# Optimization experiments

Hardware: AMD Instinct MI355X
Metric: run time of the kernel (lower is better)

Reference implementation:

```python
import jax, jax.numpy as jnp
import numpy as np

N_NODES = 100000
N_EDGES = 1600000
NODE_NF = 11   # num_node_fs
EDGE_NF = 4    # edges_nf
H_NF = 128     # h_nf
EMB_NF = 4     # emb_nf


def _linear_params(k, fan_in, fan_out):
    # torch nn.Linear default init: U(-1/sqrt(fan_in), 1/sqrt(fan_in))
    lim = 1.0 / np.sqrt(fan_in)
    kw, kb = jax.random.split(k)
    W = jax.random.uniform(kw, (fan_in, fan_out), minval=-lim, maxval=lim, dtype=jnp.float32)
    b = jax.random.uniform(kb, (fan_out,), minval=-lim, maxval=lim, dtype=jnp.float32)
    return W, b


def setup_inputs() -> dict:
    key = jax.random.key(0)
    ks = jax.random.split(key, 8)
    node_feats = jax.random.normal(ks[0], (N_NODES, NODE_NF), dtype=jnp.float32)
    edge_index = jax.random.randint(ks[1], (2, N_EDGES), 0, N_NODES, dtype=jnp.int32)
    edge_attr = jax.random.normal(ks[2], (N_EDGES, EDGE_NF), dtype=jnp.float32)
    # NELayer edge MLP: Linear(2*in_nf+edges_nf, h_nf) -> ReLU -> Linear(h_nf, h_nf) -> ReLU
    eW1, eb1 = _linear_params(ks[3], 2 * NODE_NF + EDGE_NF, H_NF)
    eW2, eb2 = _linear_params(ks[4], H_NF, H_NF)
    # NELayer node MLP: Linear(in_nf+h_nf, h_nf) -> ReLU -> Linear(h_nf, out_nf=h_nf)
    nW1, nb1 = _linear_params(ks[5], NODE_NF + H_NF, H_NF)
    nW2, nb2 = _linear_params(ks[6], H_NF, H_NF)
    # fc_emb: Linear(h_nf, emb_nf)
    fW, fb = _linear_params(ks[7], H_NF, EMB_NF)
    return dict(node_feats=node_feats, edge_index=edge_index, edge_attr=edge_attr,
                eW1=eW1, eb1=eb1, eW2=eW2, eb2=eb2,
                nW1=nW1, nb1=nb1, nW2=nW2, nb2=nb2, fW=fW, fb=fb)


def reference(node_feats, edge_index, edge_attr,
              eW1, eb1, eW2, eb2, nW1, nb1, nW2, nb2, fW, fb):
    row, col = edge_index[0], edge_index[1]          # [E], [E]
    src = node_feats[row]                            # [E, NODE_NF] gather
    dst = node_feats[col]                            # [E, NODE_NF] gather
    # edge model
    e_in = jnp.concatenate([src, dst, edge_attr], axis=1)   # [E, 2*NODE_NF+EDGE_NF]
    e_h = jax.nn.relu(e_in @ eW1 + eb1)
    edge_feats = jax.nn.relu(e_h @ eW2 + eb2)                # [E, H_NF]
    # node model: scatter-sum edge feats to source nodes
    agg = jax.ops.segment_sum(edge_feats, row, num_segments=node_feats.shape[0])  # [N, H_NF]
    n_in = jnp.concatenate([node_feats, agg], axis=1)        # [N, NODE_NF+H_NF]
    n_h = jax.nn.relu(n_in @ nW1 + nb1)
    h = n_h @ nW2 + nb2                                      # [N, H_NF]
    # embedding head
    return h @ fW + fb                                       # [N, EMB_NF]
```

## Files before the change

### kernel.cpp

```cpp
#include <hip/hip_runtime.h>

#define N_NODES 100000
#define N_EDGES 1600000
#define NODE_NF 11
#define EDGE_NF 4
#define H_NF 128
#define SCAN_B 1024
#define NBLK ((N_NODES + SCAN_B - 1) / SCAN_B)

#define K1P 40
#define K2P 136
#define EFP 131
#define K1N 160

typedef _Float16 half8 __attribute__((ext_vector_type(8)));
typedef float floatx4 __attribute__((ext_vector_type(4)));

__device__ inline half8 load8f(const float* p) {
    float4 x0 = *(const float4*)(p);
    float4 x1 = *(const float4*)(p + 4);
    half8 r;
    r[0]=(_Float16)x0.x; r[1]=(_Float16)x0.y; r[2]=(_Float16)x0.z; r[3]=(_Float16)x0.w;
    r[4]=(_Float16)x1.x; r[5]=(_Float16)x1.y; r[6]=(_Float16)x1.z; r[7]=(_Float16)x1.w;
    return r;
}
__device__ inline half8 zero8() {
    half8 z;
    #pragma unroll
    for (int j = 0; j < 8; ++j) z[j] = (_Float16)0.f;
    return z;
}

#define SEG0 (N_NODES * 12)
#define SEG1 (SEG0 + H_NF * K1P)
#define SEG2 (SEG1 + H_NF * K2P)
#define SEG3 (SEG2 + H_NF * K1N)
#define SEG4 (SEG3 + 16 * K2P + 4)
#define SEG5 (SEG4 + N_EDGES)

__global__ __launch_bounds__(256)
void prep_hist_kernel(const float* __restrict__ nf,
                      const float* __restrict__ eW1,
                      const float* __restrict__ eW2,
                      const float* __restrict__ nW1,
                      const float* __restrict__ nW2,
                      const float* __restrict__ fW,
                      const float* __restrict__ nb2,
                      const float* __restrict__ fb,
                      const int*   __restrict__ edge_index,
                      _Float16* __restrict__ nfh,
                      _Float16* __restrict__ w1h,
                      _Float16* __restrict__ w2h,
                      _Float16* __restrict__ w1nh,
                      _Float16* __restrict__ w23h,
                      float* __restrict__ b23,
                      int* hist)
{
    int i = blockIdx.x * 256 + threadIdx.x;
    if (i < SEG0) {
        int n = i / 12, k = i - n * 12;
        nfh[i] = (k < NODE_NF) ? (_Float16)nf[(size_t)n * NODE_NF + k] : (_Float16)0.f;
    } else if (i < SEG1) {
        int j = i - SEG0;
        int n = j / K1P, k = j - n * K1P;
        float v = 0.f;
        if (k < 11)                 v = eW1[k * H_NF + n];
        else if (k >= 12 && k < 23) v = eW1[(k - 1) * H_NF + n];
        else if (k >= 24 && k < 28) v = eW1[(k - 2) * H_NF + n];
        w1h[j] = (_Float16)v;
    } else if (i < SEG2) {
        int j = i - SEG1;
        int n = j / K2P, k = j - n * K2P;
        w2h[j] = (k < H_NF) ? (_Float16)eW2[k * H_NF + n] : (_Float16)0.f;
    } else if (i < SEG3) {
        int j = i - SEG2;
        int n = j / K1N, k = j - n * K1N;
        float v = 0.f;
        if (k < 11)                  v = nW1[k * H_NF + n];
        else if (k >= 12 && k < 140) v = nW1[(k - 1) * H_NF + n];
        w1nh[j] = (_Float16)v;
    } else if (i < SEG4) {
        int j = i - SEG3;
        if (j < 16 * K2P) {
            int n = j / K2P, k = j - n * K2P;
            float v = 0.f;
            if (n < 4 && k < H_NF) {
                for (int q = 0; q < H_NF; ++q) v += nW2[k * H_NF + q] * fW[q * 4 + n];
            }
            w23h[j] = (_Float16)v;
        } else {
            int o = j - 16 * K2P;
            float v = fb[o];
            for (int q = 0; q < H_NF; ++q) v += nb2[q] * fW[q * 4 + o];
            b23[o] = v;
        }
    } else if (i < SEG5) {
        int e = i - SEG4;
        atomicAdd(&hist[edge_index[e]], 1);
    }
}

__global__ __launch_bounds__(256)
void transpose_w2(const float* __restrict__ W, float* __restrict__ WT) {
    int i = blockIdx.x * 256 + threadIdx.x;
    if (i < H_NF * H_NF) {
        int k = i >> 7, j = i & (H_NF - 1);
        WT[j * H_NF + k] = W[i];
    }
}

__global__ __launch_bounds__(SCAN_B)
void scan1_kernel(const int* __restrict__ hist, int* starts, int* bsum) {
    __shared__ int buf[SCAN_B];
    int i = blockIdx.x * SCAN_B + threadIdx.x;
    int v = (i < N_NODES) ? hist[i] : 0;
    buf[threadIdx.x] = v;
    __syncthreads();
    for (int off = 1; off < SCAN_B; off <<= 1) {
        int t = (threadIdx.x >= off) ? buf[threadIdx.x - off] : 0;
        __syncthreads();
        buf[threadIdx.x] += t;
        __syncthreads();
    }
    if (i < N_NODES) starts[i] = buf[threadIdx.x] - v;
    if (threadIdx.x == SCAN_B - 1) bsum[blockIdx.x] = buf[SCAN_B - 1];
}

__global__ void scan2_kernel(int* bsum) {
    if (threadIdx.x == 0 && blockIdx.x == 0) {
        int run = 0;
        for (int b = 0; b < NBLK; ++b) { int t = bsum[b]; bsum[b] = run; run += t; }
        bsum[NBLK] = run;
    }
}

__global__ __launch_bounds__(256)
void scan3_kernel(int* starts, int* cursor, const int* __restrict__ bsum) {
    int i = blockIdx.x * 256 + threadIdx.x;
    if (i < N_NODES) {
        int s = starts[i] + bsum[i / SCAN_B];
        starts[i] = s;
        cursor[i] = s;
    }
    if (i == 0) starts[N_NODES] = bsum[NBLK];
}

__global__ __launch_bounds__(256)
void permrec_kernel(const int* __restrict__ edge_index,
                    const float* __restrict__ edge_attr,
                    int* cursor,
                    int4* __restrict__ rec)
{
    int e = blockIdx.x * 256 + threadIdx.x;
    if (e >= N_EDGES) return;
    int row = edge_index[e];
    int col = edge_index[N_EDGES + e];
    float4 a4 = ((const float4*)edge_attr)[e];
    union { _Float16 h[4]; int2 v; } u;
    u.h[0] = (_Float16)a4.x; u.h[1] = (_Float16)a4.y;
    u.h[2] = (_Float16)a4.z; u.h[3] = (_Float16)a4.w;
    int pos = atomicAdd(&cursor[row], 1);
    rec[pos] = make_int4(row, col, u.v.x, u.v.y);
}

__global__ __launch_bounds__(256)
void permute_kernel(const int* __restrict__ edge_index, int* cursor, int* perm) {
    int e = blockIdx.x * 256 + threadIdx.x;
    if (e < N_EDGES) {
        int pos = atomicAdd(&cursor[edge_index[e]], 1);
        perm[pos] = e;
    }
}

#define E_ARENA_SZ 5504

__global__ __launch_bounds__(256, 2)
void edge_mfma_kernel(const int4* __restrict__ recs,
                      const _Float16* __restrict__ nfh,
                      const _Float16* __restrict__ w1h,
                      const float* __restrict__ eb1,
                      const _Float16* __restrict__ w2h,
                      const float* __restrict__ eb2,
                      float* agg)
{
    __shared__ __align__(16) char smem[4 * E_ARENA_SZ];
    int t = threadIdx.x;
    int wv = t >> 6, lane = t & 63;
    char* arena = smem + wv * E_ARENA_SZ;
    _Float16* Ain = (_Float16*)arena;
    _Float16* Hs  = (_Float16*)(arena + 1024);
    int m = lane & 15, quad = lane >> 4;

    half8 w1f[8], w2f[8][4];
    #pragma unroll
    for (int tile = 0; tile < 8; ++tile)
        w1f[tile] = *(const half8*)(w1h + (tile * 16 + m) * K1P + quad * 8);
    #pragma unroll
    for (int tile = 0; tile < 8; ++tile)
        #pragma unroll
        for (int ks = 0; ks < 4; ++ks)
            w2f[tile][ks] = *(const half8*)(w2h + (tile * 16 + m) * K2P + ks * 32 + quad * 8);
    float b1v[8], b2v[8];
    #pragma unroll
    for (int tile = 0; tile < 8; ++tile) {
        b1v[tile] = eb1[tile * 16 + m];
        b2v[tile] = eb2[tile * 16 + m];
    }

    const int nwin = N_EDGES / 16;
    const int STRIDE = gridDim.x * 4;
    int win = blockIdx.x * 4 + wv;
    if (win >= nwin) return;

    int4 rc = recs[win * 16 + m];
    int2 g0 = make_int2(0, 0), g1 = g0, g2 = g0;
    if (quad < 2) {
        int node = (quad == 0) ? rc.x : rc.y;
        const int2* p = (const int2*)(nfh + (size_t)node * 12);
        g0 = p[0]; g1 = p[1]; g2 = p[2];
    }

    while (true) {
        int next = win + STRIDE;
        bool hn = next < nwin;
        int4 rcn = make_int4(0, 0, 0, 0);
        if (hn) rcn = recs[next * 16 + m];

        _Float16* arow = Ain + m * 32;
        if (quad == 0) {
            ((int2*)arow)[0] = g0; ((int2*)arow)[1] = g1; ((int2*)arow)[2] = g2;
        } else if (quad == 1) {
            int2* d = (int2*)(arow + 12);
            d[0] = g0; d[1] = g1; d[2] = g2;
        } else if (quad == 2) {
            int2* d = (int2*)(arow + 24);
            d[0] = make_int2(rc.z, rc.w);
            d[1] = make_int2(0, 0);
        }

        half8 a1 = *(const half8*)(Ain + m * 32 + quad * 8);

        #pragma unroll
        for (int tile = 0; tile < 8; ++tile) {
            floatx4 c = {0.f, 0.f, 0.f, 0.f};
            c = __builtin_amdgcn_mfma_f32_16x16x32_f16(a1, w1f[tile], c, 0, 0, 0);
            int n = tile * 16 + m;
            #pragma unroll
            for (int r = 0; r < 4; ++r)
                Hs[(quad * 4 + r) * K2P + n] = (_Float16)fmaxf(c[r] + b1v[tile], 0.f);
        }

        half8 a2[4];
        #pragma unroll
        for (int ks = 0; ks < 4; ++ks)
            a2[ks] = *(const half8*)(Hs + m * K2P + ks * 32 + quad * 8);

        float vals[32];
        #pragma unroll
        for (int tile = 0; tile < 8; ++tile) {
            floatx4 c = {0.f, 0.f, 0.f, 0.f};
            #pragma unroll
            for (int ks = 0; ks < 4; ++ks)
                c = __builtin_amdgcn_mfma_f32_16x16x32_f16(a2[ks], w2f[tile][ks], c, 0, 0, 0);
            #pragma unroll
            for (int r = 0; r < 4; ++r)
                vals[tile * 4 + r] = fmaxf(c[r] + b2v[tile], 0.f);
        }

        int2 n0 = make_int2(0, 0), n1 = n0, n2 = n0;
        if (hn && quad < 2) {
            int node = (quad == 0) ? rcn.x : rcn.y;
            const int2* p = (const int2*)(nfh + (size_t)node * 12);
            n0 = p[0]; n1 = p[1]; n2 = p[2];
        }

        int row = rc.x;
        int rprev = __shfl(row, lane - 1);
        bool bi = (lane < 16) && (m == 0 || rprev != row);
        unsigned long long bm = __ballot(bi);
        unsigned mk = (unsigned)(bm & 0xFFFFull);
        int er0 = __shfl(row, quad * 4 + 0);
        int er1 = __shfl(row, quad * 4 + 1);
        int er2 = __shfl(row, quad * 4 + 2);
        int er3 = __shfl(row, quad * 4 + 3);
        while (mk) {
            int start = __builtin_ctz(mk);
            mk &= mk - 1;
            int srow = __shfl(row, start);
            float s[8];
            #pragma unroll
            for (int tile = 0; tile < 8; ++tile) {
                float v = 0.f;
                if (er0 == srow) v += vals[tile * 4 + 0];
                if (er1 == srow) v += vals[tile * 4 + 1];
                if (er2 == srow) v += vals[tile * 4 + 2];
                if (er3 == srow) v += vals[tile * 4 + 3];
                s[tile] = v;
            }
            #pragma unroll
            for (int tile = 0; tile < 8; ++tile) {
                s[tile] += __shfl_xor(s[tile], 16);
                s[tile] += __shfl_xor(s[tile], 32);
            }
            if (quad == 0) {
                #pragma unroll
                for (int tile = 0; tile < 8; ++tile)
                    unsafeAtomicAdd(&agg[(size_t)srow * H_NF + tile * 16 + m], s[tile]);
            }
        }

        if (!hn) break;
        win = next; rc = rcn; g0 = n0; g1 = n1; g2 = n2;
    }
}

#define G_W1      0
#define G_W2      10240
#define G_ARENA   45056
#define G_ARENA_SZ 8448
#define G_TOTAL   (G_ARENA + 4 * G_ARENA_SZ)

__global__ __launch_bounds__(256, 2)
void edge_mfma_gather_kernel(const _Float16* __restrict__ nfh,
                             const int*   __restrict__ edge_index,
                             const float* __restrict__ edge_attr,
                             const _Float16* __restrict__ w1h,
                             const float* __restrict__ eb1,
                             const _Float16* __restrict__ w2h,
                             const float* __restrict__ eb2,
                             const int*   __restrict__ perm,
                             float* agg)
{
    __shared__ __align__(16) char smem[G_TOTAL];
    _Float16* W1s = (_Float16*)(smem + G_W1);
    _Float16* W2s = (_Float16*)(smem + G_W2);
    int t = threadIdx.x;
    {
        const float4* g1 = (const float4*)w1h;
        float4* s1 = (float4*)W1s;
        for (int i = t; i < 640; i += 256) s1[i] = g1[i];
        const float4* g2 = (const float4*)w2h;
        float4* s2 = (float4*)W2s;
        for (int i = t; i < 2176; i += 256) s2[i] = g2[i];
    }
    __syncthreads();

    int wv = t >> 6, lane = t & 63;
    char* arena = smem + G_ARENA + wv * G_ARENA_SZ;
    _Float16* Ain  = (_Float16*)arena;
    _Float16* Hs   = (_Float16*)(arena + 1280);
    float*    efS  = (float*)arena;
    int*      rowsS = (int*)(arena + 8384);

    int m = lane & 15, quad = lane >> 4;
    int el = lane & 15, grp = lane >> 4;
    _Float16* arow = Ain + el * K1P;

    float b1v[8], b2v[8];
    #pragma unroll
    for (int tile = 0; tile < 8; ++tile) {
        b1v[tile] = eb1[tile * 16 + m];
        b2v[tile] = eb2[tile * 16 + m];
    }

    const int nwin = N_EDGES / 16;
    for (int win = blockIdx.x * 4 + wv; win < nwin; win += gridDim.x * 4) {
        int e = perm[win * 16 + el];
        if (grp < 2) {
            int node = edge_index[grp * N_EDGES + e];
            const int2* p = (const int2*)(nfh + (size_t)node * 12);
            int2 x0 = p[0], x1 = p[1], x2 = p[2];
            char* dst = (char*)(arow + grp * 12);
            *(int2*)(dst) = x0; *(int2*)(dst + 8) = x1; *(int2*)(dst + 16) = x2;
        } else if (grp == 2) {
            float4 a4 = ((const float4*)edge_attr)[e];
            arow[24] = (_Float16)a4.x; arow[25] = (_Float16)a4.y;
            arow[26] = (_Float16)a4.z; arow[27] = (_Float16)a4.w;
        } else {
            rowsS[el] = edge_index[e];
            *(int2*)((char*)arow + 56) = make_int2(0, 0);
        }

        half8 a1 = *(const half8*)(Ain + m * K1P + quad * 8);
        #pragma unroll
        for (int tile = 0; tile < 8; ++tile) {
            half8 b = *(const half8*)(W1s + (tile * 16 + m) * K1P + quad * 8);
            floatx4 c = {0.f, 0.f, 0.f, 0.f};
            c = __builtin_amdgcn_mfma_f32_16x16x32_f16(a1, b, c, 0, 0, 0);
            int n = tile * 16 + m;
            #pragma unroll
            for (int r = 0; r < 4; ++r)
                Hs[(quad * 4 + r) * K2P + n] = (_Float16)fmaxf(c[r] + b1v[tile], 0.f);
        }
        half8 a2[4];
        #pragma unroll
        for (int ks = 0; ks < 4; ++ks)
            a2[ks] = *(const half8*)(Hs + m * K2P + ks * 32 + quad * 8);
        #pragma unroll
        for (int tile = 0; tile < 8; ++tile) {
            floatx4 c = {0.f, 0.f, 0.f, 0.f};
            #pragma unroll
            for (int ks = 0; ks < 4; ++ks) {
                half8 b = *(const half8*)(W2s + (tile * 16 + m) * K2P + ks * 32 + quad * 8);
                c = __builtin_amdgcn_mfma_f32_16x16x32_f16(a2[ks], b, c, 0, 0, 0);
            }
            #pragma unroll
            for (int r = 0; r < 4; ++r)
                efS[(quad * 4 + r) * EFP + tile * 16 + m] = fmaxf(c[r] + b2v[tile], 0.f);
        }

        int f = lane;
        int cur = rowsS[0];
        float acc0 = efS[f], acc1 = efS[64 + f];
        #pragma unroll 1
        for (int i = 1; i < 16; ++i) {
            int r = rowsS[i];
            float v0 = efS[i * EFP + f];
            float v1 = efS[i * EFP + 64 + f];
            if (r != cur) {
                unsafeAtomicAdd(&agg[(size_t)cur * H_NF + f], acc0);
                unsafeAtomicAdd(&agg[(size_t)cur * H_NF + 64 + f], acc1);
                acc0 = v0; acc1 = v1; cur = r;
            } else { acc0 += v0; acc1 += v1; }
        }
        unsafeAtomicAdd(&agg[(size_t)cur * H_NF + f], acc0);
        unsafeAtomicAdd(&agg[(size_t)cur * H_NF + 64 + f], acc1);
    }
}

#define N_W1    0
#define N_W23   40960
#define N_HS    45312

__global__ __launch_bounds__(256, 2)
void node_mfma_kernel(const float* __restrict__ node_feats,
                      const float* __restrict__ agg,
                      const _Float16* __restrict__ w1nh,
                      const float* __restrict__ nb1,
                      const _Float16* __restrict__ w23h,
                      const float* __restrict__ b23,
                      float* __restrict__ out)
{
    __shared__ __align__(16) char smem[N_HS + 4 * 4352];
    _Float16* W1N  = (_Float16*)(smem + N_W1);
    _Float16* W23s = (_Float16*)(smem + N_W23);
    int t = threadIdx.x;
    {
        const float4* g1 = (const float4*)w1nh;
        float4* s1 = (float4*)W1N;
        for (int i = t; i < 2560; i += 256) s1[i] = g1[i];
        const float4* g2 = (const float4*)w23h;
        float4* s2 = (float4*)W23s;
        for (int i = t; i < 272; i += 256) s2[i] = g2[i];
    }
    __syncthreads();

    int wv = t >> 6, lane = t & 63;
    int m = lane & 15, quad = lane >> 4;
    _Float16* HsW = (_Float16*)(smem + N_HS + wv * 4352);
    const int ntile = (N_NODES + 63) / 64;

    float nb1v[8];
    #pragma unroll
    for (int tile = 0; tile < 8; ++tile) nb1v[tile] = nb1[tile * 16 + m];
    float b23v = (m < 4) ? b23[m] : 0.f;

    for (int ti = blockIdx.x; ti < ntile; ti += gridDim.x) {
        int nb = (ti * 4 + wv) * 16;
        if (nb >= N_NODES) continue;
        int nodeA = nb + m;
        if (nodeA >= N_NODES) nodeA = N_NODES - 1;
        const float* ag  = agg + (size_t)nodeA * H_NF;
        const float* nfp = node_feats + (size_t)nodeA * NODE_NF;

        half8 afr[5];
        if (quad == 0) {
            half8 r;
            #pragma unroll
            for (int j = 0; j < 8; ++j) r[j] = (_Float16)nfp[j];
            afr[0] = r;
            afr[4] = load8f(ag + 116);
        } else if (quad == 1) {
            half8 r;
            r[0] = (_Float16)nfp[8]; r[1] = (_Float16)nfp[9];
            r[2] = (_Float16)nfp[10]; r[3] = (_Float16)0.f;
            float4 x = *(const float4*)(ag);
            r[4] = (_Float16)x.x; r[5] = (_Float16)x.y;
            r[6] = (_Float16)x.z; r[7] = (_Float16)x.w;
            afr[0] = r;
            float4 y = *(const float4*)(ag + 124);
            half8 s = zero8();
            s[0] = (_Float16)y.x; s[1] = (_Float16)y.y;
            s[2] = (_Float16)y.z; s[3] = (_Float16)y.w;
            afr[4] = s;
        } else if (quad == 2) {
            afr[0] = load8f(ag + 4);
            afr[4] = zero8();
        } else {
            afr[0] = load8f(ag + 12);
            afr[4] = zero8();
        }
        afr[1] = load8f(ag + 20 + 8 * quad);
        afr[2] = load8f(ag + 52 + 8 * quad);
        afr[3] = load8f(ag + 84 + 8 * quad);

        #pragma unroll
        for (int tile = 0; tile < 8; ++tile) {
            floatx4 c = {0.f, 0.f, 0.f, 0.f};
            #pragma unroll
            for (int ks = 0; ks < 5; ++ks) {
                half8 b = *(const half8*)(W1N + (tile * 16 + m) * K1N + ks * 32 + quad * 8);
                c = __builtin_amdgcn_mfma_f32_16x16x32_f16(afr[ks], b, c, 0, 0, 0);
            }
            #pragma unroll
            for (int r = 0; r < 4; ++r)
                HsW[(quad * 4 + r) * K2P + tile * 16 + m] = (_Float16)fmaxf(c[r] + nb1v[tile], 0.f);
        }

        half8 a2[4];
        #pragma unroll
        for (int ks = 0; ks < 4; ++ks)
            a2[ks] = *(const half8*)(HsW + m * K2P + ks * 32 + quad * 8);
        floatx4 c23 = {0.f, 0.f, 0.f, 0.f};
        #pragma unroll
        for (int ks = 0; ks < 4; ++ks) {
            half8 b = *(const half8*)(W23s + m * K2P + ks * 32 + quad * 8);
            c23 = __builtin_amdgcn_mfma_f32_16x16x32_f16(a2[ks], b, c23, 0, 0, 0);
        }
        if (m < 4) {
            #pragma unroll
            for (int r = 0; r < 4; ++r) {
                int node = nb + quad * 4 + r;
                if (node < N_NODES) out[node * 4 + m] = c23[r] + b23v;
            }
        }
    }
}

__global__ __launch_bounds__(256)
void edge_kernel_atomic(const float* __restrict__ node_feats,
                        const int*   __restrict__ edge_index,
                        const float* __restrict__ edge_attr,
                        const float* __restrict__ eW1,
                        const float* __restrict__ eb1,
                        const float* __restrict__ W2T,
                        const float* __restrict__ eb2,
                        float* agg)
{
    int e = blockIdx.x * 256 + threadIdx.x;
    if (e >= N_EDGES) return;
    int row = edge_index[e];
    int col = edge_index[N_EDGES + e];
    float h[H_NF];
    #pragma unroll
    for (int j = 0; j < H_NF; ++j) h[j] = eb1[j];
    const float* srcp = node_feats + (size_t)row * NODE_NF;
    #pragma unroll 1
    for (int k = 0; k < NODE_NF; ++k) {
        float x = srcp[k];
        const float* w = eW1 + k * H_NF;
        #pragma unroll
        for (int j = 0; j < H_NF; ++j) h[j] = fmaf(x, w[j], h[j]);
    }
    const float* dstp = node_feats + (size_t)col * NODE_NF;
    #pragma unroll 1
    for (int k = 0; k < NODE_NF; ++k) {
        float x = dstp[k];
        const float* w = eW1 + (NODE_NF + k) * H_NF;
        #pragma unroll
        for (int j = 0; j < H_NF; ++j) h[j] = fmaf(x, w[j], h[j]);
    }
    float4 at = ((const float4*)edge_attr)[e];
    float av[EDGE_NF] = {at.x, at.y, at.z, at.w};
    #pragma unroll
    for (int k = 0; k < EDGE_NF; ++k) {
        float x = av[k];
        const float* w = eW1 + (2 * NODE_NF + k) * H_NF;
        #pragma unroll
        for (int j = 0; j < H_NF; ++j) h[j] = fmaf(x, w[j], h[j]);
    }
    #pragma unroll
    for (int j = 0; j < H_NF; ++j) h[j] = fmaxf(h[j], 0.f);
    #pragma unroll 1
    for (int j0 = 0; j0 < H_NF; j0 += 8) {
        float acc[8];
        #pragma unroll
        for (int jj = 0; jj < 8; ++jj) acc[jj] = eb2[j0 + jj];
        #pragma unroll
        for (int k = 0; k < H_NF; ++k) {
            float x = h[k];
            #pragma unroll
            for (int jj = 0; jj < 8; ++jj)
                acc[jj] = fmaf(x, W2T[(j0 + jj) * H_NF + k], acc[jj]);
        }
        #pragma unroll
        for (int jj = 0; jj < 8; ++jj)
            unsafeAtomicAdd(&agg[(size_t)row * H_NF + j0 + jj], fmaxf(acc[jj], 0.f));
    }
}

__global__ __launch_bounds__(256)
void node_kernel1(const float* __restrict__ node_feats, float* agg_nh,
                  const float* __restrict__ nW1, const float* __restrict__ nb1)
{
    int n = blockIdx.x * 256 + threadIdx.x;
    if (n >= N_NODES) return;
    float acc[H_NF];
    #pragma unroll
    for (int j = 0; j < H_NF; ++j) acc[j] = nb1[j];
    const float* nfp = node_feats + (size_t)n * NODE_NF;
    #pragma unroll 1
    for (int k = 0; k < NODE_NF; ++k) {
        float x = nfp[k];
        const float* w = nW1 + k * H_NF;
        #pragma unroll
        for (int j = 0; j < H_NF; ++j) acc[j] = fmaf(x, w[j], acc[j]);
    }
    const float4* ap = (const float4*)(agg_nh + (size_t)n * H_NF);
    #pragma unroll 1
    for (int k4 = 0; k4 < H_NF / 4; ++k4) {
        float4 x = ap[k4];
        const float* w0 = nW1 + (NODE_NF + k4 * 4 + 0) * H_NF;
        const float* w1 = nW1 + (NODE_NF + k4 * 4 + 1) * H_NF;
        const float* w2 = nW1 + (NODE_NF + k4 * 4 + 2) * H_NF;
        const float* w3 = nW1 + (NODE_NF + k4 * 4 + 3) * H_NF;
        #pragma unroll
        for (int j = 0; j < H_NF; ++j) {
            acc[j] = fmaf(x.x, w0[j], acc[j]);
            acc[j] = fmaf(x.y, w1[j], acc[j]);
            acc[j] = fmaf(x.z, w2[j], acc[j]);
            acc[j] = fmaf(x.w, w3[j], acc[j]);
        }
    }
    float* op = agg_nh + (size_t)n * H_NF;
    #pragma unroll
    for (int j4 = 0; j4 < H_NF / 4; ++j4) {
        float4 o = make_float4(fmaxf(acc[j4*4+0], 0.f), fmaxf(acc[j4*4+1], 0.f),
                               fmaxf(acc[j4*4+2], 0.f), fmaxf(acc[j4*4+3], 0.f));
        ((float4*)op)[j4] = o;
    }
}

__global__ __launch_bounds__(256)
void node_kernel2(const float* __restrict__ nh, const float* __restrict__ nW2,
                  const float* __restrict__ nb2, const float* __restrict__ fW,
                  const float* __restrict__ fb, float* __restrict__ out)
{
    int n = blockIdx.x * 256 + threadIdx.x;
    if (n >= N_NODES) return;
    float acc[H_NF];
    #pragma unroll
    for (int j = 0; j < H_NF; ++j) acc[j] = nb2[j];
    const float4* hp = (const float4*)(nh + (size_t)n * H_NF);
    #pragma unroll 1
    for (int k4 = 0; k4 < H_NF / 4; ++k4) {
        float4 x = hp[k4];
        const float* w0 = nW2 + (k4 * 4 + 0) * H_NF;
        const float* w1 = nW2 + (k4 * 4 + 1) * H_NF;
        const float* w2 = nW2 + (k4 * 4 + 2) * H_NF;
        const float* w3 = nW2 + (k4 * 4 + 3) * H_NF;
        #pragma unroll
        for (int j = 0; j < H_NF; ++j) {
            acc[j] = fmaf(x.x, w0[j], acc[j]);
            acc[j] = fmaf(x.y, w1[j], acc[j]);
            acc[j] = fmaf(x.z, w2[j], acc[j]);
            acc[j] = fmaf(x.w, w3[j], acc[j]);
        }
    }
    float o0 = fb[0], o1 = fb[1], o2 = fb[2], o3 = fb[3];
    #pragma unroll
    for (int j = 0; j < H_NF; ++j) {
        o0 = fmaf(acc[j], fW[j * 4 + 0], o0);
        o1 = fmaf(acc[j], fW[j * 4 + 1], o1);
        o2 = fmaf(acc[j], fW[j * 4 + 2], o2);
        o3 = fmaf(acc[j], fW[j * 4 + 3], o3);
    }
    ((float4*)out)[n] = make_float4(o0, o1, o2, o3);
}

extern "C" void kernel_launch(void* const* d_in, const int* in_sizes, int n_in,
                              void* d_out, int out_size, void* d_ws, size_t ws_size,
                              hipStream_t stream)
{
    const float* node_feats = (const float*)d_in[0];
    const int*   edge_index = (const int*)d_in[1];
    const float* edge_attr  = (const float*)d_in[2];
    const float* eW1 = (const float*)d_in[3];
    const float* eb1 = (const float*)d_in[4];
    const float* eW2 = (const float*)d_in[5];
    const float* eb2 = (const float*)d_in[6];
    const float* nW1 = (const float*)d_in[7];
    const float* nb1 = (const float*)d_in[8];
    const float* nW2 = (const float*)d_in[9];
    const float* nb2 = (const float*)d_in[10];
    const float* fW  = (const float*)d_in[11];
    const float* fb  = (const float*)d_in[12];
    float* out = (float*)d_out;

    size_t off = 0;
    auto carve = [&](size_t bytes) {
        void* p = (char*)d_ws + off;
        off = (off + bytes + 255) & ~(size_t)255;
        return p;
    };
    float*     agg    = (float*)carve((size_t)N_NODES * H_NF * sizeof(float));
    int*       hist   = (int*)  carve((size_t)N_NODES * sizeof(int));
    size_t zero_bytes = off;
    int*       starts = (int*)  carve((size_t)(N_NODES + 1) * sizeof(int));
    int*       cursor = (int*)  carve((size_t)N_NODES * sizeof(int));
    int*       bsum   = (int*)  carve((size_t)(NBLK + 1) * sizeof(int));
    _Float16*  nfh    = (_Float16*)carve((size_t)N_NODES * 12 * sizeof(_Float16));
    _Float16*  w1h    = (_Float16*)carve((size_t)H_NF * K1P * sizeof(_Float16));
    _Float16*  w2h    = (_Float16*)carve((size_t)H_NF * K2P * sizeof(_Float16));
    _Float16*  w1nh   = (_Float16*)carve((size_t)H_NF * K1N * sizeof(_Float16));
    _Float16*  w23h   = (_Float16*)carve((size_t)16 * K2P * sizeof(_Float16));
    float*     b23    = (float*)carve(4 * sizeof(float));
    int*       perm   = (int*)  carve((size_t)N_EDGES * sizeof(int));
    size_t required_t2 = off;
    int4*      rec    = (int4*) carve((size_t)N_EDGES * sizeof(int4));
    size_t required_t1 = off;

    if (ws_size >= required_t2) {
        hipMemsetAsync(d_ws, 0, zero_bytes, stream);
        prep_hist_kernel<<<(SEG5 + 255) / 256, 256, 0, stream>>>(
            node_feats, eW1, eW2, nW1, nW2, fW, nb2, fb, edge_index,
            nfh, w1h, w2h, w1nh, w23h, b23, hist);
        scan1_kernel<<<NBLK, SCAN_B, 0, stream>>>(hist, starts, bsum);
        scan2_kernel<<<1, 64, 0, stream>>>(bsum);
        scan3_kernel<<<(N_NODES + 255) / 256, 256, 0, stream>>>(starts, cursor, bsum);

        if (ws_size >= required_t1) {
            permrec_kernel<<<(N_EDGES + 255) / 256, 256, 0, stream>>>(
                edge_index, edge_attr, cursor, rec);
            edge_mfma_kernel<<<512, 256, 0, stream>>>(
                rec, nfh, w1h, eb1, w2h, eb2, agg);
        } else {
            permute_kernel<<<(N_EDGES + 255) / 256, 256, 0, stream>>>(edge_index, cursor, perm);
            edge_mfma_gather_kernel<<<512, 256, 0, stream>>>(
                nfh, edge_index, edge_attr, w1h, eb1, w2h, eb2, perm, agg);
        }
        node_mfma_kernel<<<512, 256, 0, stream>>>(
            node_feats, agg, w1nh, nb1, w23h, b23, out);
    } else {
        float* agg_fb = (float*)d_ws;
        float* W2T_fb = (float*)((char*)d_ws + (size_t)N_NODES * H_NF * sizeof(float));
        transpose_w2<<<(H_NF * H_NF + 255) / 256, 256, 0, stream>>>(eW2, W2T_fb);
        hipMemsetAsync(agg_fb, 0, (size_t)N_NODES * H_NF * sizeof(float), stream);
        edge_kernel_atomic<<<(N_EDGES + 255) / 256, 256, 0, stream>>>(
            node_feats, edge_index, edge_attr, eW1, eb1, W2T_fb, eb2, agg_fb);
        node_kernel1<<<(N_NODES + 255) / 256, 256, 0, stream>>>(node_feats, agg_fb, nW1, nb1);
        node_kernel2<<<(N_NODES + 255) / 256, 256, 0, stream>>>(agg_fb, nW2, nb2, fW, fb, out);
    }
}
```

Baseline: 426.9 us.

## Split second edge-MLP layer across waves to cut registers and raise occupancy

Each wave now holds only two of the eight second-layer weight tiles. The four waves share their first-layer hidden activations through double-buffered LDS with a block barrier, and each wave computes its 32 output columns for all four windows. Fewer weight registers allow three blocks per CU and a 768-block grid. The cost is a __syncthreads per iteration, extra LDS traffic and an atomic scatter loop repeated per window.

```diff
diff --git a/kernel.cpp b/kernel.cpp
--- a/kernel.cpp
+++ b/kernel.cpp
@@ -172,9 +172,7 @@
     }
 }
 
-#define E_ARENA_SZ 5504
-
-__global__ __launch_bounds__(256, 2)
+__global__ __launch_bounds__(256, 3)
 void edge_mfma_kernel(const int4* __restrict__ recs,
                       const _Float16* __restrict__ nfh,
                       const _Float16* __restrict__ w1h,
@@ -183,88 +181,101 @@
                       const float* __restrict__ eb2,
                       float* agg)
 {
-    __shared__ __align__(16) char smem[4 * E_ARENA_SZ];
+    __shared__ __align__(16) char smem[4 * 1024 + 8 * 4352];
     int t = threadIdx.x;
     int wv = t >> 6, lane = t & 63;
-    char* arena = smem + wv * E_ARENA_SZ;
-    _Float16* Ain = (_Float16*)arena;
-    _Float16* Hs  = (_Float16*)(arena + 1024);
+    _Float16* Ain = (_Float16*)(smem + wv * 1024);
+    char* hsbase = smem + 4096;
     int m = lane & 15, quad = lane >> 4;
 
-    half8 w1f[8], w2f[8][4];
+    half8 w1f[8], w2f[2][4];
     #pragma unroll
     for (int tile = 0; tile < 8; ++tile)
         w1f[tile] = *(const half8*)(w1h + (tile * 16 + m) * K1P + quad * 8);
     #pragma unroll
-    for (int tile = 0; tile < 8; ++tile)
+    for (int tt = 0; tt < 2; ++tt)
         #pragma unroll
         for (int ks = 0; ks < 4; ++ks)
-            w2f[tile][ks] = *(const half8*)(w2h + (tile * 16 + m) * K2P + ks * 32 + quad * 8);
-    float b1v[8], b2v[8];
-    #pragma unroll
-    for (int tile = 0; tile < 8; ++tile) {
-        b1v[tile] = eb1[tile * 16 + m];
-        b2v[tile] = eb2[tile * 16 + m];
-    }
+            w2f[tt][ks] = *(const half8*)(w2h + ((wv * 2 + tt) * 16 + m) * K2P + ks * 32 + quad * 8);
+    float b1v[8], b2v[2];
+    #pragma unroll
+    for (int tile = 0; tile < 8; ++tile) b1v[tile] = eb1[tile * 16 + m];
+    #pragma unroll
+    for (int tt = 0; tt < 2; ++tt) b2v[tt] = eb2[(wv * 2 + tt) * 16 + m];
 
     const int nwin = N_EDGES / 16;
     const int STRIDE = gridDim.x * 4;
-    int win = blockIdx.x * 4 + wv;
-    if (win >= nwin) return;
-
-    int4 rc = recs[win * 16 + m];
+    int base = blockIdx.x * 4;
+    int win = base + wv;
+
+    int4 rc = make_int4(0, 0, 0, 0);
+    if (win < nwin) rc = recs[win * 16 + m];
     int2 g0 = make_int2(0, 0), g1 = g0, g2 = g0;
-    if (quad < 2) {
+    if (win < nwin && quad < 2) {
         int node = (quad == 0) ? rc.x : rc.y;
         const int2* p = (const int2*)(nfh + (size_t)node * 12);
         g0 = p[0]; g1 = p[1]; g2 = p[2];
     }
 
-    while (true) {
+    int buf = 0;
+    for (; base < nwin; base += STRIDE, win += STRIDE) {
+        bool hw = win < nwin;
         int next = win + STRIDE;
         bool hn = next < nwin;
         int4 rcn = make_int4(0, 0, 0, 0);
         if (hn) rcn = recs[next * 16 + m];
 
-        _Float16* arow = Ain + m * 32;
-        if (quad == 0) {
-            ((int2*)arow)[0] = g0; ((int2*)arow)[1] = g1; ((int2*)arow)[2] = g2;
-        } else if (quad == 1) {
-            int2* d = (int2*)(arow + 12);
-            d[0] = g0; d[1] = g1; d[2] = g2;
-        } else if (quad == 2) {
-            int2* d = (int2*)(arow + 24);
-            d[0] = make_int2(rc.z, rc.w);
-            d[1] = make_int2(0, 0);
-        }
-
-        half8 a1 = *(const half8*)(Ain + m * 32 + quad * 8);
-
-        #pragma unroll
-        for (int tile = 0; tile < 8; ++tile) {
-            floatx4 c = {0.f, 0.f, 0.f, 0.f};
-            c = __builtin_amdgcn_mfma_f32_16x16x32_f16(a1, w1f[tile], c, 0, 0, 0);
-            int n = tile * 16 + m;
-            #pragma unroll
-            for (int r = 0; r < 4; ++r)
-                Hs[(quad * 4 + r) * K2P + n] = (_Float16)fmaxf(c[r] + b1v[tile], 0.f);
-        }
-
-        half8 a2[4];
-        #pragma unroll
-        for (int ks = 0; ks < 4; ++ks)
-            a2[ks] = *(const half8*)(Hs + m * K2P + ks * 32 + quad * 8);
-
-        float vals[32];
-        #pragma unroll
-        for (int tile = 0; tile < 8; ++tile) {
-            floatx4 c = {0.f, 0.f, 0.f, 0.f};
-            #pragma unroll
-            for (int ks = 0; ks < 4; ++ks)
-                c = __builtin_amdgcn_mfma_f32_16x16x32_f16(a2[ks], w2f[tile][ks], c, 0, 0, 0);
-            #pragma unroll
-            for (int r = 0; r < 4; ++r)
-                vals[tile * 4 + r] = fmaxf(c[r] + b2v[tile], 0.f);
+        int rowj[4];
+        #pragma unroll
+        for (int j = 0; j < 4; ++j)
+            rowj[j] = (base + j < nwin) ? ((const int*)recs)[(base + j) * 64 + m * 4] : -1;
+
+        if (hw) {
+            _Float16* arow = Ain + m * 32;
+            if (quad == 0) {
+                ((int2*)arow)[0] = g0; ((int2*)arow)[1] = g1; ((int2*)arow)[2] = g2;
+            } else if (quad == 1) {
+                int2* d = (int2*)(arow + 12);
+                d[0] = g0; d[1] = g1; d[2] = g2;
+            } else if (quad == 2) {
+                int2* d = (int2*)(arow + 24);
+                d[0] = make_int2(rc.z, rc.w);
+                d[1] = make_int2(0, 0);
+            }
+            half8 a1 = *(const half8*)(Ain + m * 32 + quad * 8);
+            _Float16* Hs = (_Float16*)(hsbase + (buf * 4 + wv) * 4352);
+            #pragma unroll
+            for (int tile = 0; tile < 8; ++tile) {
+                floatx4 c = {0.f, 0.f, 0.f, 0.f};
+                c = __builtin_amdgcn_mfma_f32_16x16x32_f16(a1, w1f[tile], c, 0, 0, 0);
+                int n = tile * 16 + m;
+                #pragma unroll
+                for (int r = 0; r < 4; ++r)
+                    Hs[(quad * 4 + r) * K2P + n] = (_Float16)fmaxf(c[r] + b1v[tile], 0.f);
+            }
+        }
+        __syncthreads();
+
+        float vals[4][8];
+        #pragma unroll
+        for (int j = 0; j < 4; ++j) {
+            if (base + j < nwin) {
+                const _Float16* Hj = (const _Float16*)(hsbase + (buf * 4 + j) * 4352);
+                half8 a2[4];
+                #pragma unroll
+                for (int ks = 0; ks < 4; ++ks)
+                    a2[ks] = *(const half8*)(Hj + m * K2P + ks * 32 + quad * 8);
+                #pragma unroll
+                for (int tt = 0; tt < 2; ++tt) {
+                    floatx4 c = {0.f, 0.f, 0.f, 0.f};
+                    #pragma unroll
+                    for (int ks = 0; ks < 4; ++ks)
+                        c = __builtin_amdgcn_mfma_f32_16x16x32_f16(a2[ks], w2f[tt][ks], c, 0, 0, 0);
+                    #pragma unroll
+                    for (int r = 0; r < 4; ++r)
+                        vals[j][tt * 4 + r] = fmaxf(c[r] + b2v[tt], 0.f);
+                }
+            }
         }
 
         int2 n0 = make_int2(0, 0), n1 = n0, n2 = n0;
@@ -274,43 +285,39 @@
             n0 = p[0]; n1 = p[1]; n2 = p[2];
         }
 
-        int row = rc.x;
-        int rprev = __shfl(row, lane - 1);
-        bool bi = (lane < 16) && (m == 0 || rprev != row);
-        unsigned long long bm = __ballot(bi);
-        unsigned mk = (unsigned)(bm & 0xFFFFull);
-        int er0 = __shfl(row, quad * 4 + 0);
-        int er1 = __shfl(row, quad * 4 + 1);
-        int er2 = __shfl(row, quad * 4 + 2);
-        int er3 = __shfl(row, quad * 4 + 3);
-        while (mk) {
-            int start = __builtin_ctz(mk);
-            mk &= mk - 1;
-            int srow = __shfl(row, start);
-            float s[8];
-            #pragma unroll
-            for (int tile = 0; tile < 8; ++tile) {
-                float v = 0.f;
-                if (er0 == srow) v += vals[tile * 4 + 0];
-                if (er1 == srow) v += vals[tile * 4 + 1];
-                if (er2 == srow) v += vals[tile * 4 + 2];
-                if (er3 == srow) v += vals[tile * 4 + 3];
-                s[tile] = v;
+        #pragma unroll
+        for (int j = 0; j < 4; ++j) {
+            if (base + j < nwin) {
+                int row = rowj[j];
+                int rprev = __shfl(row, lane - 1);
+                bool bi = (lane < 16) && (m == 0 || rprev != row);
+                unsigned long long bm = __ballot(bi);
+                unsigned mk = (unsigned)(bm & 0xFFFFull);
+                int er0 = __shfl(row, quad * 4 + 0);
+                int er1 = __shfl(row, quad * 4 + 1);
+                int er2 = __shfl(row, quad * 4 + 2);
+                int er3 = __shfl(row, quad * 4 + 3);
+                while (mk) {
+                    int start = __builtin_ctz(mk);
+                    mk &= mk - 1;
+                    int srow = __shfl(row, start);
+                    float s0 = 0.f, s1 = 0.f;
+                    if (er0 == srow) { s0 += vals[j][0]; s1 += vals[j][4]; }
+                    if (er1 == srow) { s0 += vals[j][1]; s1 += vals[j][5]; }
+                    if (er2 == srow) { s0 += vals[j][2]; s1 += vals[j][6]; }
+                    if (er3 == srow) { s0 += vals[j][3]; s1 += vals[j][7]; }
+                    s0 += __shfl_xor(s0, 16); s0 += __shfl_xor(s0, 32);
+                    s1 += __shfl_xor(s1, 16); s1 += __shfl_xor(s1, 32);
+                    if (quad == 0) {
+                        unsafeAtomicAdd(&agg[(size_t)srow * H_NF + (wv * 2 + 0) * 16 + m], s0);
+                        unsafeAtomicAdd(&agg[(size_t)srow * H_NF + (wv * 2 + 1) * 16 + m], s1);
+                    }
+                }
             }
-            #pragma unroll
-            for (int tile = 0; tile < 8; ++tile) {
-                s[tile] += __shfl_xor(s[tile], 16);
-                s[tile] += __shfl_xor(s[tile], 32);
-            }
-            if (quad == 0) {
-                #pragma unroll
-                for (int tile = 0; tile < 8; ++tile)
-                    unsafeAtomicAdd(&agg[(size_t)srow * H_NF + tile * 16 + m], s[tile]);
-            }
-        }
-
-        if (!hn) break;
-        win = next; rc = rcn; g0 = n0; g1 = n1; g2 = n2;
+        }
+
+        rc = rcn; g0 = n0; g1 = n1; g2 = n2;
+        buf ^= 1;
     }
 }
 
@@ -732,7 +739,7 @@
         if (ws_size >= required_t1) {
             permrec_kernel<<<(N_EDGES + 255) / 256, 256, 0, stream>>>(
                 edge_index, edge_attr, cursor, rec);
-            edge_mfma_kernel<<<512, 256, 0, stream>>>(
+            edge_mfma_kernel<<<768, 256, 0, stream>>>(
                 rec, nfh, w1h, eb1, w2h, eb2, agg);
         } else {
             permute_kernel<<<(N_EDGES + 255) / 256, 256, 0, stream>>>(edge_index, cursor, perm);
```

Result: slower. 447.1 us (+4.7%).

## Keep edge MLP hidden layer in registers via transposed MFMA and permuted W2

Applied to the files above, without the earlier changes.

The edge kernel now builds the first-layer A operand with lane shuffles instead of staging through LDS. It computes the first GEMM transposed so each lane's output already matches the second MFMA's A-fragment layout, which drops the LDS round-trip and frees shared memory. To make this work, eW2's K dimension is permuted at prep time and eb1 is folded into the W1 matrix as an extra column multiplied by a constant 1.0. The fallback gather kernel's A-fragment loads are changed to match the permuted W2, and the bias in fp16 adds slight precision risk.

```diff
diff --git a/kernel.cpp b/kernel.cpp
--- a/kernel.cpp
+++ b/kernel.cpp
@@ -41,6 +41,7 @@
 __global__ __launch_bounds__(256)
 void prep_hist_kernel(const float* __restrict__ nf,
                       const float* __restrict__ eW1,
+                      const float* __restrict__ eb1,
                       const float* __restrict__ eW2,
                       const float* __restrict__ nW1,
                       const float* __restrict__ nW2,
@@ -67,11 +68,18 @@
         if (k < 11)                 v = eW1[k * H_NF + n];
         else if (k >= 12 && k < 23) v = eW1[(k - 1) * H_NF + n];
         else if (k >= 24 && k < 28) v = eW1[(k - 2) * H_NF + n];
+        else if (k == 28)           v = eb1[n];
         w1h[j] = (_Float16)v;
     } else if (i < SEG2) {
         int j = i - SEG1;
         int n = j / K2P, k = j - n * K2P;
-        w2h[j] = (k < H_NF) ? (_Float16)eW2[k * H_NF + n] : (_Float16)0.f;
+        float v = 0.f;
+        if (k < H_NF) {
+            int ks = k >> 5, rem = k & 31, q = rem >> 3, jj = rem & 7;
+            int ka = ks * 32 + ((jj >> 2) << 4) + q * 4 + (jj & 3);
+            v = eW2[ka * H_NF + n];
+        }
+        w2h[j] = (_Float16)v;
     } else if (i < SEG3) {
         int j = i - SEG2;
         int n = j / K1N, k = j - n * K1N;
@@ -172,23 +180,16 @@
     }
 }
 
-#define E_ARENA_SZ 5504
-
 __global__ __launch_bounds__(256, 2)
 void edge_mfma_kernel(const int4* __restrict__ recs,
                       const _Float16* __restrict__ nfh,
                       const _Float16* __restrict__ w1h,
-                      const float* __restrict__ eb1,
                       const _Float16* __restrict__ w2h,
                       const float* __restrict__ eb2,
                       float* agg)
 {
-    __shared__ __align__(16) char smem[4 * E_ARENA_SZ];
     int t = threadIdx.x;
     int wv = t >> 6, lane = t & 63;
-    char* arena = smem + wv * E_ARENA_SZ;
-    _Float16* Ain = (_Float16*)arena;
-    _Float16* Hs  = (_Float16*)(arena + 1024);
     int m = lane & 15, quad = lane >> 4;
 
     half8 w1f[8], w2f[8][4];
@@ -200,12 +201,10 @@
         #pragma unroll
         for (int ks = 0; ks < 4; ++ks)
             w2f[tile][ks] = *(const half8*)(w2h + (tile * 16 + m) * K2P + ks * 32 + quad * 8);
-    float b1v[8], b2v[8];
-    #pragma unroll
-    for (int tile = 0; tile < 8; ++tile) {
-        b1v[tile] = eb1[tile * 16 + m];
+    float b2v[8];
+    #pragma unroll
+    for (int tile = 0; tile < 8; ++tile)
         b2v[tile] = eb2[tile * 16 + m];
-    }
 
     const int nwin = N_EDGES / 16;
     const int STRIDE = gridDim.x * 4;
@@ -226,34 +225,30 @@
         int4 rcn = make_int4(0, 0, 0, 0);
         if (hn) rcn = recs[next * 16 + m];
 
-        _Float16* arow = Ain + m * 32;
-        if (quad == 0) {
-            ((int2*)arow)[0] = g0; ((int2*)arow)[1] = g1; ((int2*)arow)[2] = g2;
-        } else if (quad == 1) {
-            int2* d = (int2*)(arow + 12);
-            d[0] = g0; d[1] = g1; d[2] = g2;
-        } else if (quad == 2) {
-            int2* d = (int2*)(arow + 24);
-            d[0] = make_int2(rc.z, rc.w);
-            d[1] = make_int2(0, 0);
-        }
-
-        half8 a1 = *(const half8*)(Ain + m * 32 + quad * 8);
-
+        int sAx = __shfl(g2.x, m),      sAy = __shfl(g2.y, m);
+        int sBx = __shfl(g1.x, m + 16), sBy = __shfl(g1.y, m + 16);
+        int sCx = __shfl(g2.x, m + 16), sCy = __shfl(g2.y, m + 16);
+        int d0 = (quad == 0) ? g0.x : (quad == 1) ? sAx : (quad == 2) ? sBx : rc.z;
+        int d1 = (quad == 0) ? g0.y : (quad == 1) ? sAy : (quad == 2) ? sBy : rc.w;
+        int d2 = (quad == 0) ? g1.x : (quad == 1) ? g0.x : (quad == 2) ? sCx : 0x00003C00;
+        int d3 = (quad == 0) ? g1.y : (quad == 1) ? g0.y : (quad == 2) ? sCy : 0;
+        union { int i[4]; half8 h; } ua;
+        ua.i[0] = d0; ua.i[1] = d1; ua.i[2] = d2; ua.i[3] = d3;
+        half8 a1 = ua.h;
+
+        union { unsigned u[4]; half8 h; } ua2[4];
         #pragma unroll
         for (int tile = 0; tile < 8; ++tile) {
             floatx4 c = {0.f, 0.f, 0.f, 0.f};
-            c = __builtin_amdgcn_mfma_f32_16x16x32_f16(a1, w1f[tile], c, 0, 0, 0);
-            int n = tile * 16 + m;
-            #pragma unroll
-            for (int r = 0; r < 4; ++r)
-                Hs[(quad * 4 + r) * K2P + n] = (_Float16)fmaxf(c[r] + b1v[tile], 0.f);
-        }
-
-        half8 a2[4];
-        #pragma unroll
-        for (int ks = 0; ks < 4; ++ks)
-            a2[ks] = *(const half8*)(Hs + m * K2P + ks * 32 + quad * 8);
+            c = __builtin_amdgcn_mfma_f32_16x16x32_f16(w1f[tile], a1, c, 0, 0, 0);
+            union { _Float16 f[2]; unsigned u; } p0, p1;
+            p0.f[0] = (_Float16)fmaxf(c[0], 0.f);
+            p0.f[1] = (_Float16)fmaxf(c[1], 0.f);
+            p1.f[0] = (_Float16)fmaxf(c[2], 0.f);
+            p1.f[1] = (_Float16)fmaxf(c[3], 0.f);
+            ua2[tile >> 1].u[(tile & 1) * 2 + 0] = p0.u;
+            ua2[tile >> 1].u[(tile & 1) * 2 + 1] = p1.u;
+        }
 
         float vals[32];
         #pragma unroll
@@ -261,7 +256,7 @@
             floatx4 c = {0.f, 0.f, 0.f, 0.f};
             #pragma unroll
             for (int ks = 0; ks < 4; ++ks)
-                c = __builtin_amdgcn_mfma_f32_16x16x32_f16(a2[ks], w2f[tile][ks], c, 0, 0, 0);
+                c = __builtin_amdgcn_mfma_f32_16x16x32_f16(ua2[ks].h, w2f[tile][ks], c, 0, 0, 0);
             #pragma unroll
             for (int r = 0; r < 4; ++r)
                 vals[tile * 4 + r] = fmaxf(c[r] + b2v[tile], 0.f);
@@ -394,8 +389,13 @@
         }
         half8 a2[4];
         #pragma unroll
-        for (int ks = 0; ks < 4; ++ks)
-            a2[ks] = *(const half8*)(Hs + m * K2P + ks * 32 + quad * 8);
+        for (int ks = 0; ks < 4; ++ks) {
+            const _Float16* hp = Hs + m * K2P + ks * 32 + quad * 4;
+            union { int2 d[2]; half8 h; } uu;
+            uu.d[0] = *(const int2*)(hp);
+            uu.d[1] = *(const int2*)(hp + 16);
+            a2[ks] = uu.h;
+        }
         #pragma unroll
         for (int tile = 0; tile < 8; ++tile) {
             floatx4 c = {0.f, 0.f, 0.f, 0.f};
@@ -723,7 +723,7 @@
     if (ws_size >= required_t2) {
         hipMemsetAsync(d_ws, 0, zero_bytes, stream);
         prep_hist_kernel<<<(SEG5 + 255) / 256, 256, 0, stream>>>(
-            node_feats, eW1, eW2, nW1, nW2, fW, nb2, fb, edge_index,
+            node_feats, eW1, eb1, eW2, nW1, nW2, fW, nb2, fb, edge_index,
             nfh, w1h, w2h, w1nh, w23h, b23, hist);
         scan1_kernel<<<NBLK, SCAN_B, 0, stream>>>(hist, starts, bsum);
         scan2_kernel<<<1, 64, 0, stream>>>(bsum);
@@ -733,7 +733,7 @@
             permrec_kernel<<<(N_EDGES + 255) / 256, 256, 0, stream>>>(
                 edge_index, edge_attr, cursor, rec);
             edge_mfma_kernel<<<512, 256, 0, stream>>>(
-                rec, nfh, w1h, eb1, w2h, eb2, agg);
+                rec, nfh, w1h, w2h, eb2, agg);
         } else {
             permute_kernel<<<(N_EDGES + 255) / 256, 256, 0, stream>>>(edge_index, cursor, perm);
             edge_mfma_gather_kernel<<<512, 256, 0, stream>>>(
```

Result: faster. 412.5 us (-3.4%).
